# Performance work log

Measured on AMD Instinct MI355X. Metric: run time of the kernel, lower is better.

The kernel has to match this reference:

```python
import jax, jax.numpy as jnp
import numpy as np

N_OSC = 256
BATCH = 1024
DT = 0.1
STEPS = 10


def setup_inputs() -> dict:
    key = jax.random.key(0)
    k_theta, k_K, k_omega = jax.random.split(key, 3)
    theta_init = jax.random.normal(k_theta, (BATCH, N_OSC), dtype=jnp.float32)
    K0 = jax.random.normal(k_K, (N_OSC, N_OSC), dtype=jnp.float32) * 0.1
    K = (K0 + K0.T) / 2  # symmetric coupling matrix, as in torch init
    omega = jax.random.normal(k_omega, (N_OSC,), dtype=jnp.float32) * 0.1
    K_global = jnp.float32(0.5)
    return {"theta_init": theta_init, "K": K, "omega": omega, "K_global": K_global}


def reference(theta_init, K, omega, K_global):
    n = K.shape[0]

    def step(theta, _):
        # diff[b, i, j] = theta[b, j] - theta[b, i]
        diff = theta[..., None, :] - theta[..., :, None]
        coupling_sum = jnp.sum(K * jnp.sin(diff), axis=-1)  # (batch, n)
        dtheta = omega + (K_global / n) * coupling_sum
        theta_new = theta + DT * dtheta
        # wrap to (-pi, pi]
        theta_new = jnp.arctan2(jnp.sin(theta_new), jnp.cos(theta_new))
        return theta_new, None

    theta, _ = jax.lax.scan(step, theta_init, None, length=STEPS)
    cos_mean = jnp.cos(theta).mean(axis=-1)
    sin_mean = jnp.sin(theta).mean(axis=-1)
    coherence = jnp.sqrt(cos_mean ** 2 + sin_mean ** 2)
    return theta, coherence
```

## Files before the change

### kernel.cpp

```cpp
#include <hip/hip_runtime.h>
#include <math.h>


typedef __attribute__((ext_vector_type(4))) float f32x4;
typedef __attribute__((ext_vector_type(2))) long long2_t;

constexpr int N       = 256;
constexpr int RB      = 16;
constexpr int STEPS   = 10;
constexpr int WAVES   = 8;
constexpr int THREADS = WAVES * 64;
constexpr float DT    = 0.1f;
constexpr float TWO_PI     = 6.28318530717958648f;
constexpr float INV_TWO_PI = 0.15915494309189535f;

__global__ __launch_bounds__(512)
void pack_k(const float* __restrict__ Kmat, unsigned char* __restrict__ kf8)
{
    const int id   = blockIdx.x * blockDim.x + threadIdx.x;
    const int T    = id >> 9;
    const int c    = (id >> 6) & 7;
    const int lane = id & 63;
    const int q    = lane >> 4, l15 = lane & 15;
    const float* src = Kmat + (size_t)(16 * T + l15) * N + 32 * c + 8 * q;
    float4 lo = *(const float4*)src;
    float4 hi = *(const float4*)(src + 4);
    int w0 = __builtin_amdgcn_cvt_pk_fp8_f32(lo.x, lo.y, 0, false);
    w0     = __builtin_amdgcn_cvt_pk_fp8_f32(lo.z, lo.w, w0, true);
    int w1 = __builtin_amdgcn_cvt_pk_fp8_f32(hi.x, hi.y, 0, false);
    w1     = __builtin_amdgcn_cvt_pk_fp8_f32(hi.z, hi.w, w1, true);
    int2 out; out.x = w0; out.y = w1;
    *(int2*)(kf8 + (size_t)id * 8) = out;
}

__global__ __launch_bounds__(THREADS, 2)
void kuramoto_r9(const float* __restrict__ theta0,
                 const unsigned char* __restrict__ kf8,
                 const float* __restrict__ omega,
                 const float* __restrict__ kglob,
                 float* __restrict__ theta_out,
                 float* __restrict__ coh_out)
{
    __shared__ __align__(16) unsigned char SC[2][RB * 512];
    __shared__ float redS[RB][WAVES], redC[RB][WAVES];

    const int tid  = threadIdx.x;
    const int wv   = tid >> 6;
    const int lane = tid & 63;
    const int q    = lane >> 4;
    const int l15  = lane & 15;
    const int b0   = blockIdx.x * RB;

    const float kgn = kglob[0] * (1.0f / 256.0f);

    long kf[2][8];
#pragma unroll
    for (int t = 0; t < 2; ++t) {
        const unsigned char* base = kf8 + (size_t)((2 * wv + t) * 512 + lane) * 8;
#pragma unroll
        for (int c = 0; c < 8; ++c)
            kf[t][c] = *(const long*)(base + (size_t)c * 512);
    }

    float th[8], om[8], sn[8], cs[8];
#pragma unroll
    for (int t = 0; t < 2; ++t) {
        const int ob = 32 * wv + 16 * t + 4 * q;
        float4 t4 = *(const float4*)(theta0 + (size_t)(b0 + l15) * N + ob);
        float4 o4 = *(const float4*)(omega + ob);
        th[4*t+0] = t4.x; th[4*t+1] = t4.y; th[4*t+2] = t4.z; th[4*t+3] = t4.w;
        om[4*t+0] = o4.x; om[4*t+1] = o4.y; om[4*t+2] = o4.z; om[4*t+3] = o4.w;
    }
#pragma unroll
    for (int k = 0; k < 8; ++k)
        __sincosf(th[k], &sn[k], &cs[k]);

    const int so = 4 * (q & 1);
    const int g0 = 4 * wv + (q >> 1);

    for (int s = 0; s < STEPS; ++s) {
        unsigned char* rowp = &SC[s & 1][l15 * 512];
#pragma unroll
        for (int t = 0; t < 2; ++t) {
            int spk = __builtin_amdgcn_cvt_pk_fp8_f32(sn[4*t+0], sn[4*t+1], 0, false);
            spk     = __builtin_amdgcn_cvt_pk_fp8_f32(sn[4*t+2], sn[4*t+3], spk, true);
            int cpk = __builtin_amdgcn_cvt_pk_fp8_f32(cs[4*t+0], cs[4*t+1], 0, false);
            cpk     = __builtin_amdgcn_cvt_pk_fp8_f32(cs[4*t+2], cs[4*t+3], cpk, true);
            const int base = (((g0 + 2 * t) ^ l15) << 4);
            *(int*)(rowp + base + so)     = spk;
            *(int*)(rowp + base + 8 + so) = cpk;
        }
        __syncthreads();

        f32x4 aS[2], aC[2];
        aS[0] = (f32x4){0.f,0.f,0.f,0.f}; aS[1] = (f32x4){0.f,0.f,0.f,0.f};
        aC[0] = (f32x4){0.f,0.f,0.f,0.f}; aC[1] = (f32x4){0.f,0.f,0.f,0.f};
#pragma unroll
        for (int c = 0; c < 8; ++c) {
            long2_t v = *(const long2_t*)(rowp + ((((4 * c + q) ^ l15)) << 4));
            aS[0] = __builtin_amdgcn_mfma_f32_16x16x32_fp8_fp8(kf[0][c], v.x, aS[0], 0, 0, 0);
            aC[0] = __builtin_amdgcn_mfma_f32_16x16x32_fp8_fp8(kf[0][c], v.y, aC[0], 0, 0, 0);
            aS[1] = __builtin_amdgcn_mfma_f32_16x16x32_fp8_fp8(kf[1][c], v.x, aS[1], 0, 0, 0);
            aC[1] = __builtin_amdgcn_mfma_f32_16x16x32_fp8_fp8(kf[1][c], v.y, aC[1], 0, 0, 0);
        }

#pragma unroll
        for (int t = 0; t < 2; ++t)
#pragma unroll
            for (int r = 0; r < 4; ++r) {
                const int k = 4 * t + r;
                float coup = cs[k] * aS[t][r] - sn[k] * aC[t][r];
                float d  = DT * fmaf(kgn, coup, om[k]);
                float d2 = d * d;
                float sd = d * fmaf(d2, -1.0f / 6.0f, 1.0f);
                float cd = fmaf(d2, fmaf(d2, 1.0f / 24.0f, -0.5f), 1.0f);
                float s2 = fmaf(sn[k], cd,  cs[k] * sd);
                float c2 = fmaf(cs[k], cd, -sn[k] * sd);
                sn[k] = s2; cs[k] = c2; th[k] += d;
            }
    }

    float ps = 0.f, pc = 0.f;
#pragma unroll
    for (int t = 0; t < 2; ++t) {
        const int ob = 32 * wv + 16 * t + 4 * q;
        float4 outv;
        outv.x = fmaf(-TWO_PI, rintf(th[4*t+0] * INV_TWO_PI), th[4*t+0]);
        outv.y = fmaf(-TWO_PI, rintf(th[4*t+1] * INV_TWO_PI), th[4*t+1]);
        outv.z = fmaf(-TWO_PI, rintf(th[4*t+2] * INV_TWO_PI), th[4*t+2]);
        outv.w = fmaf(-TWO_PI, rintf(th[4*t+3] * INV_TWO_PI), th[4*t+3]);
        *(float4*)(theta_out + (size_t)(b0 + l15) * N + ob) = outv;
#pragma unroll
        for (int r = 0; r < 4; ++r) { ps += sn[4*t+r]; pc += cs[4*t+r]; }
    }
    ps += __shfl_xor(ps, 16, 64);  pc += __shfl_xor(pc, 16, 64);
    ps += __shfl_xor(ps, 32, 64);  pc += __shfl_xor(pc, 32, 64);
    if (q == 0) { redS[l15][wv] = ps; redC[l15][wv] = pc; }
    __syncthreads();
    if (tid < RB) {
        float S = 0.f, C = 0.f;
#pragma unroll
        for (int k = 0; k < WAVES; ++k) { S += redS[tid][k]; C += redC[tid][k]; }
        float sm = S * (1.0f / 256.0f);
        float cm = C * (1.0f / 256.0f);
        coh_out[b0 + tid] = sqrtf(sm * sm + cm * cm);
    }
}

extern "C" void kernel_launch(void* const* d_in, const int* in_sizes, int n_in,
                              void* d_out, int out_size, void* d_ws, size_t ws_size,
                              hipStream_t stream) {
    const float* theta0 = (const float*)d_in[0];
    const float* Kmat   = (const float*)d_in[1];
    const float* omega  = (const float*)d_in[2];
    const float* kglob  = (const float*)d_in[3];

    unsigned char* kf8 = (unsigned char*)d_ws;

    float* theta_out = (float*)d_out;
    float* coh_out   = theta_out + 1024 * N;

    pack_k<<<dim3(16), dim3(512), 0, stream>>>(Kmat, kf8);
    kuramoto_r9<<<dim3(1024 / RB), dim3(THREADS), 0, stream>>>(
        theta0, kf8, omega, kglob, theta_out, coh_out);
}
```

Baseline: 71.41 us.

## Fuse K fp8 packing into main kernel via shared memory staging

Removes the separate pack_k launch. Each block now reads the full fp32 K matrix, converts it to fp8 and stores it in shared memory in the MFMA fragment layout, then loads its register fragments from LDS. This drops one kernel launch and the workspace round trip. In exchange every one of the 64 blocks redundantly reads 256KB of K and converts it, and uses 64KB more LDS, which may limit occupancy to fewer blocks per CU.

```diff
diff --git a/kernel.cpp b/kernel.cpp
--- a/kernel.cpp
+++ b/kernel.cpp
@@ -14,33 +14,15 @@
 constexpr float TWO_PI     = 6.28318530717958648f;
 constexpr float INV_TWO_PI = 0.15915494309189535f;
 
-__global__ __launch_bounds__(512)
-void pack_k(const float* __restrict__ Kmat, unsigned char* __restrict__ kf8)
+__global__ __launch_bounds__(THREADS, 2)
+void kuramoto_r10(const float* __restrict__ theta0,
+                  const float* __restrict__ Kmat,
+                  const float* __restrict__ omega,
+                  const float* __restrict__ kglob,
+                  float* __restrict__ theta_out,
+                  float* __restrict__ coh_out)
 {
-    const int id   = blockIdx.x * blockDim.x + threadIdx.x;
-    const int T    = id >> 9;
-    const int c    = (id >> 6) & 7;
-    const int lane = id & 63;
-    const int q    = lane >> 4, l15 = lane & 15;
-    const float* src = Kmat + (size_t)(16 * T + l15) * N + 32 * c + 8 * q;
-    float4 lo = *(const float4*)src;
-    float4 hi = *(const float4*)(src + 4);
-    int w0 = __builtin_amdgcn_cvt_pk_fp8_f32(lo.x, lo.y, 0, false);
-    w0     = __builtin_amdgcn_cvt_pk_fp8_f32(lo.z, lo.w, w0, true);
-    int w1 = __builtin_amdgcn_cvt_pk_fp8_f32(hi.x, hi.y, 0, false);
-    w1     = __builtin_amdgcn_cvt_pk_fp8_f32(hi.z, hi.w, w1, true);
-    int2 out; out.x = w0; out.y = w1;
-    *(int2*)(kf8 + (size_t)id * 8) = out;
-}
-
-__global__ __launch_bounds__(THREADS, 2)
-void kuramoto_r9(const float* __restrict__ theta0,
-                 const unsigned char* __restrict__ kf8,
-                 const float* __restrict__ omega,
-                 const float* __restrict__ kglob,
-                 float* __restrict__ theta_out,
-                 float* __restrict__ coh_out)
-{
+    __shared__ __align__(16) unsigned char KF[N * N];
     __shared__ __align__(16) unsigned char SC[2][RB * 512];
     __shared__ float redS[RB][WAVES], redC[RB][WAVES];
 
@@ -53,15 +35,6 @@
 
     const float kgn = kglob[0] * (1.0f / 256.0f);
 
-    long kf[2][8];
-#pragma unroll
-    for (int t = 0; t < 2; ++t) {
-        const unsigned char* base = kf8 + (size_t)((2 * wv + t) * 512 + lane) * 8;
-#pragma unroll
-        for (int c = 0; c < 8; ++c)
-            kf[t][c] = *(const long*)(base + (size_t)c * 512);
-    }
-
     float th[8], om[8], sn[8], cs[8];
 #pragma unroll
     for (int t = 0; t < 2; ++t) {
@@ -71,9 +44,38 @@
         th[4*t+0] = t4.x; th[4*t+1] = t4.y; th[4*t+2] = t4.z; th[4*t+3] = t4.w;
         om[4*t+0] = o4.x; om[4*t+1] = o4.y; om[4*t+2] = o4.z; om[4*t+3] = o4.w;
     }
+
+#pragma unroll 4
+    for (int i = 0; i < 16; ++i) {
+        const int g   = i * THREADS + tid;
+        const int row = g >> 5;
+        const int u8  = g & 31;
+        const float* src = Kmat + (size_t)g * 8;
+        float4 lo = *(const float4*)src;
+        float4 hi = *(const float4*)(src + 4);
+        int w0 = __builtin_amdgcn_cvt_pk_fp8_f32(lo.x, lo.y, 0, false);
+        w0     = __builtin_amdgcn_cvt_pk_fp8_f32(lo.z, lo.w, w0, true);
+        int w1 = __builtin_amdgcn_cvt_pk_fp8_f32(hi.x, hi.y, 0, false);
+        w1     = __builtin_amdgcn_cvt_pk_fp8_f32(hi.z, hi.w, w1, true);
+        const int id = ((row >> 4) << 9) | ((u8 >> 2) << 6) | ((u8 & 3) << 4) | (row & 15);
+        int2 outp; outp.x = w0; outp.y = w1;
+        *(int2*)(KF + (size_t)id * 8) = outp;
+    }
+
 #pragma unroll
     for (int k = 0; k < 8; ++k)
         __sincosf(th[k], &sn[k], &cs[k]);
+
+    __syncthreads();
+
+    long kf[2][8];
+#pragma unroll
+    for (int t = 0; t < 2; ++t) {
+        const unsigned char* base = KF + (size_t)((2 * wv + t) * 512 + lane) * 8;
+#pragma unroll
+        for (int c = 0; c < 8; ++c)
+            kf[t][c] = *(const long*)(base + (size_t)c * 512);
+    }
 
     const int so = 4 * (q & 1);
     const int g0 = 4 * wv + (q >> 1);
@@ -155,12 +157,11 @@
     const float* omega  = (const float*)d_in[2];
     const float* kglob  = (const float*)d_in[3];
 
-    unsigned char* kf8 = (unsigned char*)d_ws;
+    (void)d_ws; (void)ws_size;
 
     float* theta_out = (float*)d_out;
     float* coh_out   = theta_out + 1024 * N;
 
-    pack_k<<<dim3(16), dim3(512), 0, stream>>>(Kmat, kf8);
-    kuramoto_r9<<<dim3(1024 / RB), dim3(THREADS), 0, stream>>>(
-        theta0, kf8, omega, kglob, theta_out, coh_out);
+    kuramoto_r10<<<dim3(1024 / RB), dim3(THREADS), 0, stream>>>(
+        theta0, Kmat, omega, kglob, theta_out, coh_out);
 }
```

Result: no change. 72.59 us (+1.6%).
